# Performance work log

Measured on AMD Instinct MI355X. Metric: run time of the kernel, lower is better.

## Reference

```python
import jax, jax.numpy as jnp
import numpy as np

N_NODES = 50000
N_EDGES = 800000
NFEAT = 256
NHID = 128
NCLASS = 40
NLAYERS = 3


def setup_inputs() -> dict:
    key = jax.random.key(0)
    ks = jax.random.split(key, 8)
    x = jax.random.normal(ks[0], (N_NODES, NFEAT), dtype=jnp.float32)
    edge_src = jax.random.randint(ks[1], (N_EDGES,), 0, N_NODES, dtype=jnp.int32)
    edge_dst = jax.random.randint(ks[2], (N_EDGES,), 0, N_NODES, dtype=jnp.int32)
    # Kaiming-ish scaled params
    W_in = jax.random.normal(ks[3], (NFEAT, NHID), dtype=jnp.float32) / np.sqrt(NFEAT)
    b_in = jnp.zeros((NHID,), dtype=jnp.float32)
    W_mlps = jax.random.normal(ks[4], (NLAYERS, NHID, NHID), dtype=jnp.float32) / np.sqrt(NHID)
    b_mlps = jnp.zeros((NLAYERS, NHID), dtype=jnp.float32)
    W_out = jax.random.normal(ks[5], (NHID, NCLASS), dtype=jnp.float32) / np.sqrt(NHID)
    b_out = jnp.zeros((NCLASS,), dtype=jnp.float32)
    return {"x": x, "edge_src": edge_src, "edge_dst": edge_dst,
            "W_in": W_in, "b_in": b_in, "W_mlps": W_mlps, "b_mlps": b_mlps,
            "W_out": W_out, "b_out": b_out}


def reference(x, edge_src, edge_dst, W_in, b_in, W_mlps, b_mlps, W_out, b_out):
    # Dropout is identity in eval mode (training=False).
    n = x.shape[0]
    h = jax.nn.relu(x @ W_in + b_in)                       # [N, H]
    for i in range(NLAYERS):
        # GINConv with eps=0: h' = h + sum_{(s->d) in E} h[s] scattered to d
        agg = jax.ops.segment_sum(h[edge_src], edge_dst, num_segments=n)
        h = jax.nn.relu((h + agg) @ W_mlps[i] + b_mlps[i])  # [N, H]
    logits = h @ W_out + b_out                              # [N, C]
    return jax.nn.log_softmax(logits, axis=1)
```

## Files before the change

kernel.cpp:

```cpp
#include <hip/hip_runtime.h>
#include <math.h>

#define NHID 128
#define NFEAT 256
#define NCLASS 40

typedef __bf16 bf16x8 __attribute__((ext_vector_type(8)));
typedef __bf16 bf16x4 __attribute__((ext_vector_type(4)));
typedef float floatx4 __attribute__((ext_vector_type(4)));


__global__ __launch_bounds__(256) void bucket_hist(const int* __restrict__ edst,
                                                   int* __restrict__ bucket_counts,
                                                   int E, int nbuck) {
    __shared__ int lh[256];
    int tid = threadIdx.x;
    lh[tid] = 0;
    __syncthreads();
    int base = blockIdx.x * 4096;
#pragma unroll
    for (int k = 0; k < 16; ++k) {
        int e = base + k * 256 + tid;
        if (e < E) atomicAdd(&lh[edst[e] >> 8], 1);
    }
    __syncthreads();
    if (tid < nbuck && lh[tid]) atomicAdd(&bucket_counts[tid], lh[tid]);
}

__global__ __launch_bounds__(256) void bucket_scan(const int* __restrict__ counts,
                                                   int* __restrict__ start,
                                                   int* __restrict__ cursor,
                                                   int* __restrict__ row_ptr,
                                                   int nbuck, int E, int N) {
    __shared__ int lds[256];
    int tid = threadIdx.x;
    int v = (tid < nbuck) ? counts[tid] : 0;
    lds[tid] = v;
    __syncthreads();
    for (int off = 1; off < 256; off <<= 1) {
        int t = (tid >= off) ? lds[tid - off] : 0;
        __syncthreads();
        lds[tid] += t;
        __syncthreads();
    }
    int excl = lds[tid] - v;
    if (tid < nbuck) { start[tid] = excl; cursor[tid] = excl; }
    if (tid == 0) { start[nbuck] = E; row_ptr[N] = E; }
}

__global__ __launch_bounds__(256) void bucket_scatter(const int* __restrict__ esrc,
                                                      const int* __restrict__ edst,
                                                      int* __restrict__ cursor,
                                                      unsigned int* __restrict__ bdata,
                                                      int E, int nbuck) {
    __shared__ int lh[256];
    __shared__ int lbase[256];
    int tid = threadIdx.x;
    lh[tid] = 0;
    __syncthreads();
    int base = blockIdx.x * 4096;
    unsigned int recs[16];
    short bks[16];
    short lofs[16];
#pragma unroll
    for (int k = 0; k < 16; ++k) {
        int e = base + k * 256 + tid;
        bks[k] = -1;
        if (e < E) {
            int d = edst[e];
            int s = esrc[e];
            int b = d >> 8;
            recs[k] = ((unsigned int)(d & 255) << 16) | (unsigned int)s;
            bks[k] = (short)b;
            lofs[k] = (short)atomicAdd(&lh[b], 1);
        }
    }
    __syncthreads();
    if (tid < nbuck && lh[tid]) lbase[tid] = atomicAdd(&cursor[tid], lh[tid]);
    __syncthreads();
#pragma unroll
    for (int k = 0; k < 16; ++k) {
        if (bks[k] >= 0) bdata[lbase[bks[k]] + lofs[k]] = recs[k];
    }
}

__global__ __launch_bounds__(256) void bucket_finalize(const unsigned int* __restrict__ bdata,
                                                       const int* __restrict__ start,
                                                       int* __restrict__ row_ptr,
                                                       int* __restrict__ srcs,
                                                       int N) {
    __shared__ int hist[256];
    __shared__ int cur[256];
    int b = blockIdx.x;
    int tid = threadIdx.x;
    int s0 = start[b];
    int cnt = start[b + 1] - s0;
    hist[tid] = 0;
    __syncthreads();
    for (int i = tid; i < cnt; i += 256) atomicAdd(&hist[bdata[s0 + i] >> 16], 1);
    __syncthreads();
    int v0 = hist[tid];
    __syncthreads();
    for (int off = 1; off < 256; off <<= 1) {
        int t = (tid >= off) ? hist[tid - off] : 0;
        __syncthreads();
        hist[tid] += t;
        __syncthreads();
    }
    int excl = hist[tid] - v0;
    cur[tid] = excl;
    int node = b * 256 + tid;
    if (node < N) row_ptr[node] = s0 + excl;
    __syncthreads();
    for (int i = tid; i < cnt; i += 256) {
        unsigned int r = bdata[s0 + i];
        int p = atomicAdd(&cur[r >> 16], 1);
        srcs[s0 + p] = (int)(r & 0xffffu);
    }
}

template <int K>
__global__ __launch_bounds__(256) void transpose_split(const float* __restrict__ src,
                                                       __bf16* __restrict__ dhi,
                                                       __bf16* __restrict__ dlo, int total) {
    int i = blockIdx.x * 256 + threadIdx.x;
    if (i >= total) return;
    int per = 128 * K;
    int l = i / per;
    int r = i - l * per;
    int n = r / K;
    int k = r - n * K;
    float v = src[(size_t)l * per + (size_t)k * 128 + n];
    __bf16 hi = (__bf16)v;
    dhi[i] = hi;
    dlo[i] = (__bf16)(v - (float)hi);
}

__global__ __launch_bounds__(256) void aggregate_fused(const __bf16* __restrict__ hhi,
                                                       const __bf16* __restrict__ hlo,
                                                       const int* __restrict__ row_ptr,
                                                       const int* __restrict__ srcs,
                                                       __bf16* __restrict__ ohi,
                                                       __bf16* __restrict__ olo, int N) {
    int tid = threadIdx.x;
    int node = blockIdx.x * 4 + (tid >> 6);
    if (node >= N) return;
    int lane = tid & 63;
    int g = lane >> 4;
    int c = lane & 15;
    int beg = row_ptr[node];
    int end = row_ptr[node + 1];
    const bf16x8* hv = (const bf16x8*)hhi;

    bf16x8 sh = hv[(size_t)node * 16 + c];
    bf16x8 sl = ((const bf16x8*)hlo)[(size_t)node * 16 + c];

    float a[8], b2[8];
#pragma unroll
    for (int j = 0; j < 8; ++j) { a[j] = 0.f; b2[j] = 0.f; }

    int i = beg;
    for (; i + 16 <= end; i += 16) {
        int s0 = __builtin_nontemporal_load(&srcs[i + g]);
        int s1 = __builtin_nontemporal_load(&srcs[i + 4 + g]);
        int s2 = __builtin_nontemporal_load(&srcs[i + 8 + g]);
        int s3 = __builtin_nontemporal_load(&srcs[i + 12 + g]);
        bf16x8 v0 = hv[(size_t)s0 * 16 + c];
        bf16x8 v1 = hv[(size_t)s1 * 16 + c];
        bf16x8 v2 = hv[(size_t)s2 * 16 + c];
        bf16x8 v3 = hv[(size_t)s3 * 16 + c];
#pragma unroll
        for (int j = 0; j < 8; ++j) {
            a[j] += (float)v0[j] + (float)v2[j];
            b2[j] += (float)v1[j] + (float)v3[j];
        }
    }
    for (; i + 8 <= end; i += 8) {
        int s0 = __builtin_nontemporal_load(&srcs[i + g]);
        int s1 = __builtin_nontemporal_load(&srcs[i + 4 + g]);
        bf16x8 v0 = hv[(size_t)s0 * 16 + c];
        bf16x8 v1 = hv[(size_t)s1 * 16 + c];
#pragma unroll
        for (int j = 0; j < 8; ++j) { a[j] += (float)v0[j]; b2[j] += (float)v1[j]; }
    }
    for (; i < end; i += 4) {
        if (i + g < end) {
            int s = __builtin_nontemporal_load(&srcs[i + g]);
            bf16x8 v = hv[(size_t)s * 16 + c];
#pragma unroll
            for (int j = 0; j < 8; ++j) a[j] += (float)v[j];
        }
    }
#pragma unroll
    for (int j = 0; j < 8; ++j) a[j] += b2[j];
#pragma unroll
    for (int j = 0; j < 8; ++j) a[j] += __shfl_xor(a[j], 16);
#pragma unroll
    for (int j = 0; j < 8; ++j) a[j] += __shfl_xor(a[j], 32);

    if (g == 0) {
        bf16x8 whi, wlo;
#pragma unroll
        for (int j = 0; j < 8; ++j) {
            float v = a[j] + (float)sh[j] + (float)sl[j];
            __bf16 h = (__bf16)v;
            whi[j] = h;
            wlo[j] = (__bf16)(v - (float)h);
        }
        ((bf16x8*)ohi)[(size_t)node * 16 + c] = whi;
        ((bf16x8*)olo)[(size_t)node * 16 + c] = wlo;
    }
}

template <int MODE>
__global__ __launch_bounds__(256) void gemm_mfma(
    const float* __restrict__ Af, const __bf16* __restrict__ Ahi,
    const __bf16* __restrict__ Alo,
    const __bf16* __restrict__ Wthi, const __bf16* __restrict__ Wtlo,
    const float* __restrict__ bias, __bf16* __restrict__ Ohi,
    __bf16* __restrict__ Olo, int M, int K) {
    __shared__ __align__(16) char smem[49152];
    __bf16* sAhi = (__bf16*)smem;
    __bf16* sAlo = (__bf16*)(smem + 8192);
    __bf16* sWhi = (__bf16*)(smem + 16384);
    __bf16* sWlo = (__bf16*)(smem + 32768);

    int tid = threadIdx.x;
    int row0 = blockIdx.x * 64;
    int wave = tid >> 6;
    int l = tid & 63;
    int m16 = l & 15;
    int q = l >> 4;
    int axor = m16 & 7;
    int arow = wave * 16 + m16;

    floatx4 acc[8];
#pragma unroll
    for (int t = 0; t < 8; ++t) acc[t] = (floatx4){0.f, 0.f, 0.f, 0.f};

    for (int k0 = 0; k0 < K; k0 += 64) {
#pragma unroll
        for (int it = 0; it < 2; ++it) {
            int lin = it * 2048 + tid * 8;
            int row = lin >> 6, k = lin & 63;
            int g = min(row0 + row, M - 1);
            int off = row * 64 + (((k >> 3) ^ (row & 7)) << 3);
            if (MODE == 0) {
                float4 v0 = *(const float4*)&Af[(size_t)g * K + k0 + k];
                float4 v1 = *(const float4*)&Af[(size_t)g * K + k0 + k + 4];
                float s[8] = {v0.x, v0.y, v0.z, v0.w, v1.x, v1.y, v1.z, v1.w};
                bf16x8 shi, slo;
#pragma unroll
                for (int j = 0; j < 8; ++j) {
                    __bf16 h = (__bf16)s[j];
                    shi[j] = h;
                    slo[j] = (__bf16)(s[j] - (float)h);
                }
                *(bf16x8*)(sAhi + off) = shi;
                *(bf16x8*)(sAlo + off) = slo;
            } else {
                *(bf16x8*)(sAhi + off) = *(const bf16x8*)&Ahi[(size_t)g * 128 + k0 + k];
                *(bf16x8*)(sAlo + off) = *(const bf16x8*)&Alo[(size_t)g * 128 + k0 + k];
            }
        }
#pragma unroll
        for (int it = 0; it < 4; ++it) {
            int lin = it * 2048 + tid * 8;
            int n = lin >> 6, kk = lin & 63;
            int off = n * 64 + (((kk >> 3) ^ (n & 7)) << 3);
            *(bf16x8*)(sWhi + off) = *(const bf16x8*)&Wthi[(size_t)n * K + k0 + kk];
            *(bf16x8*)(sWlo + off) = *(const bf16x8*)&Wtlo[(size_t)n * K + k0 + kk];
        }
        __syncthreads();

#pragma unroll
        for (int s = 0; s < 2; ++s) {
            int sw = (((s * 4 + q) ^ axor) << 3);
            bf16x8 ahi = *(bf16x8*)(sAhi + arow * 64 + sw);
            bf16x8 alo = *(bf16x8*)(sAlo + arow * 64 + sw);
#pragma unroll
            for (int t = 0; t < 8; ++t) {
                int n = t * 16 + m16;
                bf16x8 bhi = *(bf16x8*)(sWhi + n * 64 + sw);
                bf16x8 blo = *(bf16x8*)(sWlo + n * 64 + sw);
                acc[t] = __builtin_amdgcn_mfma_f32_16x16x32_bf16(ahi, bhi, acc[t], 0, 0, 0);
                acc[t] = __builtin_amdgcn_mfma_f32_16x16x32_bf16(alo, bhi, acc[t], 0, 0, 0);
                acc[t] = __builtin_amdgcn_mfma_f32_16x16x32_bf16(ahi, blo, acc[t], 0, 0, 0);
            }
        }
        __syncthreads();
    }

    float* eps = (float*)(smem + 16384);
#pragma unroll
    for (int t = 0; t < 8; ++t) {
        int col = t * 16 + m16;
        float bb = bias[col];
#pragma unroll
        for (int i = 0; i < 4; ++i) {
            int row = wave * 16 + q * 4 + i;
            eps[row * 128 + col] = fmaxf(acc[t][i] + bb, 0.f);
        }
    }
    __syncthreads();
#pragma unroll
    for (int it = 0; it < 8; ++it) {
        int lin = it * 1024 + tid * 4;
        int row = lin >> 7, col = lin & 127;
        int g = row0 + row;
        if (g < M) {
            float4 v = *(float4*)(eps + lin);
            bf16x4 hi, lo;
            float vv[4] = {v.x, v.y, v.z, v.w};
#pragma unroll
            for (int j = 0; j < 4; ++j) {
                __bf16 h = (__bf16)vv[j];
                hi[j] = h;
                lo[j] = (__bf16)(vv[j] - (float)h);
            }
            *(bf16x4*)&Ohi[(size_t)g * 128 + col] = hi;
            *(bf16x4*)&Olo[(size_t)g * 128 + col] = lo;
        }
    }
}

__global__ __launch_bounds__(256) void out_logsoftmax(const __bf16* __restrict__ hhi,
                                                      const __bf16* __restrict__ hlo,
                                                      const float* __restrict__ Wout,
                                                      const float* __restrict__ bout,
                                                      float* __restrict__ out, int M) {
    __shared__ float sW[128 * NCLASS];
    __shared__ float sb[NCLASS];
    __shared__ float sH[32 * 132];
    int tid = threadIdx.x;
    for (int i = tid; i < 128 * NCLASS; i += 256) sW[i] = Wout[i];
    if (tid < NCLASS) sb[tid] = bout[tid];
    int row0 = blockIdx.x * 32;
#pragma unroll
    for (int it = 0; it < 4; ++it) {
        int i = tid * 4 + it * 1024;
        int r = i >> 7, k = i & 127;
        int rr = min(row0 + r, M - 1);
        uint2 uh = *(const uint2*)&hhi[(size_t)rr * 128 + k];
        uint2 ul = *(const uint2*)&hlo[(size_t)rr * 128 + k];
        sH[r * 132 + k + 0] = __uint_as_float(uh.x << 16) + __uint_as_float(ul.x << 16);
        sH[r * 132 + k + 1] = __uint_as_float(uh.x & 0xffff0000u) + __uint_as_float(ul.x & 0xffff0000u);
        sH[r * 132 + k + 2] = __uint_as_float(uh.y << 16) + __uint_as_float(ul.y << 16);
        sH[r * 132 + k + 3] = __uint_as_float(uh.y & 0xffff0000u) + __uint_as_float(ul.y & 0xffff0000u);
    }
    __syncthreads();

    int r = tid >> 3;
    int cg = tid & 7;
    float z[5];
#pragma unroll
    for (int j = 0; j < 5; ++j) z[j] = sb[cg * 5 + j];
    for (int k = 0; k < 128; ++k) {
        float a = sH[r * 132 + k];
#pragma unroll
        for (int j = 0; j < 5; ++j) z[j] += a * sW[k * NCLASS + cg * 5 + j];
    }
    float m = z[0];
#pragma unroll
    for (int j = 1; j < 5; ++j) m = fmaxf(m, z[j]);
    for (int off = 1; off < 8; off <<= 1) m = fmaxf(m, __shfl_xor(m, off));
    float s = 0.f;
#pragma unroll
    for (int j = 0; j < 5; ++j) s += expf(z[j] - m);
    for (int off = 1; off < 8; off <<= 1) s += __shfl_xor(s, off);
    float lse = m + logf(s);
    int row = row0 + r;
    if (row < M) {
#pragma unroll
        for (int j = 0; j < 5; ++j) out[(size_t)row * NCLASS + cg * 5 + j] = z[j] - lse;
    }
}

extern "C" void kernel_launch(void* const* d_in, const int* in_sizes, int n_in,
                              void* d_out, int out_size, void* d_ws, size_t ws_size,
                              hipStream_t stream) {
    const float* x      = (const float*)d_in[0];
    const int*   esrc   = (const int*)d_in[1];
    const int*   edst   = (const int*)d_in[2];
    const float* W_in   = (const float*)d_in[3];
    const float* b_in   = (const float*)d_in[4];
    const float* W_mlps = (const float*)d_in[5];
    const float* b_mlps = (const float*)d_in[6];
    const float* W_out  = (const float*)d_in[7];
    const float* b_out  = (const float*)d_in[8];
    float* out = (float*)d_out;

    int N = in_sizes[0] / NFEAT;
    int E = in_sizes[1];
    int nbuck = (N + 255) >> 8;

    char* ws = (char*)d_ws;
    size_t hb = (((size_t)N * NHID * sizeof(__bf16)) + 255) & ~(size_t)255;
    __bf16* h_hi_a = (__bf16*)ws;
    __bf16* h_lo_a = (__bf16*)(ws + hb);
    __bf16* h_hi_b = (__bf16*)(ws + 2 * hb);
    __bf16* h_lo_b = (__bf16*)(ws + 3 * hb);
    __bf16* sum_hi = (__bf16*)(ws + 4 * hb);
    __bf16* sum_lo = (__bf16*)(ws + 5 * hb);
    unsigned int* bdata = (unsigned int*)(ws + 4 * hb);
    char* ip = ws + 6 * hb;
    int* row_ptr = (int*)ip;  ip += (((size_t)(N + 1) * 4) + 255) & ~(size_t)255;
    int* srcs    = (int*)ip;  ip += (((size_t)E * 4) + 255) & ~(size_t)255;
    int* bucket_counts = (int*)ip;  ip += 1024;
    int* bucket_start  = (int*)ip;  ip += 1024;
    int* bucket_cursor = (int*)ip;  ip += 1024;
    __bf16* Wt_in_hi   = (__bf16*)ip;  ip += 128 * NFEAT * 2;
    __bf16* Wt_in_lo   = (__bf16*)ip;  ip += 128 * NFEAT * 2;
    __bf16* Wt_mlps_hi = (__bf16*)ip;  ip += 3 * 128 * NHID * 2;
    __bf16* Wt_mlps_lo = (__bf16*)ip;  ip += 3 * 128 * NHID * 2;

    int eb4 = (E + 4095) / 4096;

    hipMemsetAsync(bucket_counts, 0, 1024, stream);
    bucket_hist<<<eb4, 256, 0, stream>>>(edst, bucket_counts, E, nbuck);
    bucket_scan<<<1, 256, 0, stream>>>(bucket_counts, bucket_start, bucket_cursor,
                                       row_ptr, nbuck, E, N);
    bucket_scatter<<<eb4, 256, 0, stream>>>(esrc, edst, bucket_cursor, bdata, E, nbuck);
    bucket_finalize<<<nbuck, 256, 0, stream>>>(bdata, bucket_start, row_ptr, srcs, N);

    transpose_split<NFEAT><<<(128 * NFEAT + 255) / 256, 256, 0, stream>>>(
        W_in, Wt_in_hi, Wt_in_lo, 128 * NFEAT);
    transpose_split<NHID><<<(3 * 128 * NHID + 255) / 256, 256, 0, stream>>>(
        W_mlps, Wt_mlps_hi, Wt_mlps_lo, 3 * 128 * NHID);

    int gb = (N + 63) / 64;
    gemm_mfma<0><<<gb, 256, 0, stream>>>(x, (const __bf16*)nullptr, (const __bf16*)nullptr,
                                         Wt_in_hi, Wt_in_lo, b_in, h_hi_a, h_lo_a, N, NFEAT);

    __bf16* cur_hi = h_hi_a; __bf16* cur_lo = h_lo_a;
    __bf16* nxt_hi = h_hi_b; __bf16* nxt_lo = h_lo_b;
    for (int i = 0; i < 3; ++i) {
        aggregate_fused<<<(N + 3) / 4, 256, 0, stream>>>(cur_hi, cur_lo, row_ptr, srcs,
                                                         sum_hi, sum_lo, N);
        gemm_mfma<1><<<gb, 256, 0, stream>>>(
            (const float*)nullptr, sum_hi, sum_lo,
            Wt_mlps_hi + (size_t)i * 128 * NHID, Wt_mlps_lo + (size_t)i * 128 * NHID,
            b_mlps + (size_t)i * NHID, nxt_hi, nxt_lo, N, NHID);
        __bf16* t;
        t = cur_hi; cur_hi = nxt_hi; nxt_hi = t;
        t = cur_lo; cur_lo = nxt_lo; nxt_lo = t;
    }

    out_logsoftmax<<<(N + 31) / 32, 256, 0, stream>>>(cur_hi, cur_lo, W_out, b_out, out, N);
}
```

Measured before the change: 330.3 us.

## Fuse neighbor aggregation into MLP GEMM per 64-row block

Merges the per-layer aggregation kernel and the MFMA GEMM into one kernel. Each block first gathers and sums neighbor features for its 64 nodes straight into shared memory as hi/lo bf16, then runs the split-bf16 GEMM with bias and ReLU. This removes the intermediate sum buffer round-trip through global memory and one launch per layer. The cost is 64KB of shared memory per block, which lowers occupancy. It also changes the gather's parallelism from 4 nodes per block to 64 nodes processed sequentially, 16 per wave, which may expose gather latency.

```diff
diff --git a/kernel.cpp b/kernel.cpp
--- a/kernel.cpp
+++ b/kernel.cpp
@@ -136,86 +136,184 @@
     dlo[i] = (__bf16)(v - (float)hi);
 }
 
-__global__ __launch_bounds__(256) void aggregate_fused(const __bf16* __restrict__ hhi,
-                                                       const __bf16* __restrict__ hlo,
-                                                       const int* __restrict__ row_ptr,
-                                                       const int* __restrict__ srcs,
-                                                       __bf16* __restrict__ ohi,
-                                                       __bf16* __restrict__ olo, int N) {
-    int tid = threadIdx.x;
-    int node = blockIdx.x * 4 + (tid >> 6);
-    if (node >= N) return;
+__global__ __launch_bounds__(256) void gin_layer_fused(
+    const __bf16* __restrict__ hhi, const __bf16* __restrict__ hlo,
+    const int* __restrict__ row_ptr, const int* __restrict__ srcs,
+    const __bf16* __restrict__ Wthi, const __bf16* __restrict__ Wtlo,
+    const float* __restrict__ bias, __bf16* __restrict__ Ohi,
+    __bf16* __restrict__ Olo, int N) {
+    __shared__ __align__(16) char smem[65536];
+    __bf16* sAhi = (__bf16*)smem;
+    __bf16* sAlo = (__bf16*)(smem + 16384);
+    __bf16* sWhi = (__bf16*)(smem + 32768);
+    __bf16* sWlo = (__bf16*)(smem + 49152);
+
+    int tid = threadIdx.x;
+    int wave = tid >> 6;
     int lane = tid & 63;
+    int row0 = blockIdx.x * 64;
+
     int g = lane >> 4;
     int c = lane & 15;
-    int beg = row_ptr[node];
-    int end = row_ptr[node + 1];
     const bf16x8* hv = (const bf16x8*)hhi;
 
-    bf16x8 sh = hv[(size_t)node * 16 + c];
-    bf16x8 sl = ((const bf16x8*)hlo)[(size_t)node * 16 + c];
-
-    float a[8], b2[8];
-#pragma unroll
-    for (int j = 0; j < 8; ++j) { a[j] = 0.f; b2[j] = 0.f; }
-
-    int i = beg;
-    for (; i + 16 <= end; i += 16) {
-        int s0 = __builtin_nontemporal_load(&srcs[i + g]);
-        int s1 = __builtin_nontemporal_load(&srcs[i + 4 + g]);
-        int s2 = __builtin_nontemporal_load(&srcs[i + 8 + g]);
-        int s3 = __builtin_nontemporal_load(&srcs[i + 12 + g]);
-        bf16x8 v0 = hv[(size_t)s0 * 16 + c];
-        bf16x8 v1 = hv[(size_t)s1 * 16 + c];
-        bf16x8 v2 = hv[(size_t)s2 * 16 + c];
-        bf16x8 v3 = hv[(size_t)s3 * 16 + c];
-#pragma unroll
-        for (int j = 0; j < 8; ++j) {
-            a[j] += (float)v0[j] + (float)v2[j];
-            b2[j] += (float)v1[j] + (float)v3[j];
-        }
-    }
-    for (; i + 8 <= end; i += 8) {
-        int s0 = __builtin_nontemporal_load(&srcs[i + g]);
-        int s1 = __builtin_nontemporal_load(&srcs[i + 4 + g]);
-        bf16x8 v0 = hv[(size_t)s0 * 16 + c];
-        bf16x8 v1 = hv[(size_t)s1 * 16 + c];
-#pragma unroll
-        for (int j = 0; j < 8; ++j) { a[j] += (float)v0[j]; b2[j] += (float)v1[j]; }
-    }
-    for (; i < end; i += 4) {
-        if (i + g < end) {
-            int s = __builtin_nontemporal_load(&srcs[i + g]);
-            bf16x8 v = hv[(size_t)s * 16 + c];
-#pragma unroll
-            for (int j = 0; j < 8; ++j) a[j] += (float)v[j];
-        }
-    }
-#pragma unroll
-    for (int j = 0; j < 8; ++j) a[j] += b2[j];
-#pragma unroll
-    for (int j = 0; j < 8; ++j) a[j] += __shfl_xor(a[j], 16);
-#pragma unroll
-    for (int j = 0; j < 8; ++j) a[j] += __shfl_xor(a[j], 32);
-
-    if (g == 0) {
-        bf16x8 whi, wlo;
-#pragma unroll
-        for (int j = 0; j < 8; ++j) {
-            float v = a[j] + (float)sh[j] + (float)sl[j];
-            __bf16 h = (__bf16)v;
-            whi[j] = h;
-            wlo[j] = (__bf16)(v - (float)h);
-        }
-        ((bf16x8*)ohi)[(size_t)node * 16 + c] = whi;
-        ((bf16x8*)olo)[(size_t)node * 16 + c] = wlo;
-    }
-}
-
-template <int MODE>
-__global__ __launch_bounds__(256) void gemm_mfma(
-    const float* __restrict__ Af, const __bf16* __restrict__ Ahi,
-    const __bf16* __restrict__ Alo,
+    int rpl = 0;
+    {
+        int idx = row0 + wave * 16 + lane;
+        if (lane <= 16 && idx <= N) rpl = row_ptr[idx];
+    }
+
+    for (int t = 0; t < 16; ++t) {
+        int r = wave * 16 + t;
+        int node = row0 + r;
+        int off = r * 128 + ((c >> 3) << 6) + (((c & 7) ^ (r & 7)) << 3);
+        if (node >= N) {
+            if (g == 0) {
+                bf16x8 z;
+#pragma unroll
+                for (int j = 0; j < 8; ++j) z[j] = (__bf16)0.f;
+                *(bf16x8*)(sAhi + off) = z;
+                *(bf16x8*)(sAlo + off) = z;
+            }
+            continue;
+        }
+        int beg = __shfl(rpl, t);
+        int end = __shfl(rpl, t + 1);
+
+        bf16x8 sh = hv[(size_t)node * 16 + c];
+        bf16x8 sl = ((const bf16x8*)hlo)[(size_t)node * 16 + c];
+
+        float a[8], b2[8];
+#pragma unroll
+        for (int j = 0; j < 8; ++j) { a[j] = 0.f; b2[j] = 0.f; }
+
+        int i = beg;
+        for (; i + 16 <= end; i += 16) {
+            int s0 = __builtin_nontemporal_load(&srcs[i + g]);
+            int s1 = __builtin_nontemporal_load(&srcs[i + 4 + g]);
+            int s2 = __builtin_nontemporal_load(&srcs[i + 8 + g]);
+            int s3 = __builtin_nontemporal_load(&srcs[i + 12 + g]);
+            bf16x8 v0 = hv[(size_t)s0 * 16 + c];
+            bf16x8 v1 = hv[(size_t)s1 * 16 + c];
+            bf16x8 v2 = hv[(size_t)s2 * 16 + c];
+            bf16x8 v3 = hv[(size_t)s3 * 16 + c];
+#pragma unroll
+            for (int j = 0; j < 8; ++j) {
+                a[j] += (float)v0[j] + (float)v2[j];
+                b2[j] += (float)v1[j] + (float)v3[j];
+            }
+        }
+        for (; i + 8 <= end; i += 8) {
+            int s0 = __builtin_nontemporal_load(&srcs[i + g]);
+            int s1 = __builtin_nontemporal_load(&srcs[i + 4 + g]);
+            bf16x8 v0 = hv[(size_t)s0 * 16 + c];
+            bf16x8 v1 = hv[(size_t)s1 * 16 + c];
+#pragma unroll
+            for (int j = 0; j < 8; ++j) { a[j] += (float)v0[j]; b2[j] += (float)v1[j]; }
+        }
+        for (; i < end; i += 4) {
+            if (i + g < end) {
+                int s = __builtin_nontemporal_load(&srcs[i + g]);
+                bf16x8 v = hv[(size_t)s * 16 + c];
+#pragma unroll
+                for (int j = 0; j < 8; ++j) a[j] += (float)v[j];
+            }
+        }
+#pragma unroll
+        for (int j = 0; j < 8; ++j) a[j] += b2[j];
+#pragma unroll
+        for (int j = 0; j < 8; ++j) a[j] += __shfl_xor(a[j], 16);
+#pragma unroll
+        for (int j = 0; j < 8; ++j) a[j] += __shfl_xor(a[j], 32);
+
+        if (g == 0) {
+            bf16x8 whi, wlo;
+#pragma unroll
+            for (int j = 0; j < 8; ++j) {
+                float v = a[j] + (float)sh[j] + (float)sl[j];
+                __bf16 h = (__bf16)v;
+                whi[j] = h;
+                wlo[j] = (__bf16)(v - (float)h);
+            }
+            *(bf16x8*)(sAhi + off) = whi;
+            *(bf16x8*)(sAlo + off) = wlo;
+        }
+    }
+    __syncthreads();
+
+    int m16 = lane & 15;
+    int q = lane >> 4;
+    int axor = m16 & 7;
+    int arow = wave * 16 + m16;
+
+    floatx4 acc[8];
+#pragma unroll
+    for (int t = 0; t < 8; ++t) acc[t] = (floatx4){0.f, 0.f, 0.f, 0.f};
+
+    for (int k0 = 0; k0 < 128; k0 += 64) {
+#pragma unroll
+        for (int it = 0; it < 4; ++it) {
+            int lin = it * 2048 + tid * 8;
+            int n = lin >> 6, kk = lin & 63;
+            int off = n * 64 + (((kk >> 3) ^ (n & 7)) << 3);
+            *(bf16x8*)(sWhi + off) = *(const bf16x8*)&Wthi[(size_t)n * 128 + k0 + kk];
+            *(bf16x8*)(sWlo + off) = *(const bf16x8*)&Wtlo[(size_t)n * 128 + k0 + kk];
+        }
+        __syncthreads();
+
+#pragma unroll
+        for (int s = 0; s < 2; ++s) {
+            int sw = (((s * 4 + q) ^ axor) << 3);
+            bf16x8 ahi = *(bf16x8*)(sAhi + arow * 128 + k0 + sw);
+            bf16x8 alo = *(bf16x8*)(sAlo + arow * 128 + k0 + sw);
+#pragma unroll
+            for (int t = 0; t < 8; ++t) {
+                int n = t * 16 + m16;
+                bf16x8 bhi = *(bf16x8*)(sWhi + n * 64 + sw);
+                bf16x8 blo = *(bf16x8*)(sWlo + n * 64 + sw);
+                acc[t] = __builtin_amdgcn_mfma_f32_16x16x32_bf16(ahi, bhi, acc[t], 0, 0, 0);
+                acc[t] = __builtin_amdgcn_mfma_f32_16x16x32_bf16(alo, bhi, acc[t], 0, 0, 0);
+                acc[t] = __builtin_amdgcn_mfma_f32_16x16x32_bf16(ahi, blo, acc[t], 0, 0, 0);
+            }
+        }
+        __syncthreads();
+    }
+
+    float* eps = (float*)(smem + 32768);
+#pragma unroll
+    for (int t = 0; t < 8; ++t) {
+        int col = t * 16 + m16;
+        float bb = bias[col];
+#pragma unroll
+        for (int i = 0; i < 4; ++i) {
+            int row = wave * 16 + q * 4 + i;
+            eps[row * 128 + col] = fmaxf(acc[t][i] + bb, 0.f);
+        }
+    }
+    __syncthreads();
+#pragma unroll
+    for (int it = 0; it < 8; ++it) {
+        int lin = it * 1024 + tid * 4;
+        int row = lin >> 7, col = lin & 127;
+        int gg = row0 + row;
+        if (gg < N) {
+            float4 v = *(float4*)(eps + lin);
+            bf16x4 hi, lo;
+            float vv[4] = {v.x, v.y, v.z, v.w};
+#pragma unroll
+            for (int j = 0; j < 4; ++j) {
+                __bf16 h = (__bf16)vv[j];
+                hi[j] = h;
+                lo[j] = (__bf16)(vv[j] - (float)h);
+            }
+            *(bf16x4*)&Ohi[(size_t)gg * 128 + col] = hi;
+            *(bf16x4*)&Olo[(size_t)gg * 128 + col] = lo;
+        }
+    }
+}
+
+__global__ __launch_bounds__(256) void gemm_in(
+    const float* __restrict__ Af,
     const __bf16* __restrict__ Wthi, const __bf16* __restrict__ Wtlo,
     const float* __restrict__ bias, __bf16* __restrict__ Ohi,
     __bf16* __restrict__ Olo, int M, int K) {
@@ -245,23 +343,18 @@
             int row = lin >> 6, k = lin & 63;
             int g = min(row0 + row, M - 1);
             int off = row * 64 + (((k >> 3) ^ (row & 7)) << 3);
-            if (MODE == 0) {
-                float4 v0 = *(const float4*)&Af[(size_t)g * K + k0 + k];
-                float4 v1 = *(const float4*)&Af[(size_t)g * K + k0 + k + 4];
-                float s[8] = {v0.x, v0.y, v0.z, v0.w, v1.x, v1.y, v1.z, v1.w};
-                bf16x8 shi, slo;
-#pragma unroll
-                for (int j = 0; j < 8; ++j) {
-                    __bf16 h = (__bf16)s[j];
-                    shi[j] = h;
-                    slo[j] = (__bf16)(s[j] - (float)h);
-                }
-                *(bf16x8*)(sAhi + off) = shi;
-                *(bf16x8*)(sAlo + off) = slo;
-            } else {
-                *(bf16x8*)(sAhi + off) = *(const bf16x8*)&Ahi[(size_t)g * 128 + k0 + k];
-                *(bf16x8*)(sAlo + off) = *(const bf16x8*)&Alo[(size_t)g * 128 + k0 + k];
-            }
+            float4 v0 = *(const float4*)&Af[(size_t)g * K + k0 + k];
+            float4 v1 = *(const float4*)&Af[(size_t)g * K + k0 + k + 4];
+            float s[8] = {v0.x, v0.y, v0.z, v0.w, v1.x, v1.y, v1.z, v1.w};
+            bf16x8 shi, slo;
+#pragma unroll
+            for (int j = 0; j < 8; ++j) {
+                __bf16 h = (__bf16)s[j];
+                shi[j] = h;
+                slo[j] = (__bf16)(s[j] - (float)h);
+            }
+            *(bf16x8*)(sAhi + off) = shi;
+            *(bf16x8*)(sAlo + off) = slo;
         }
 #pragma unroll
         for (int it = 0; it < 4; ++it) {
@@ -400,8 +493,6 @@
     __bf16* h_lo_a = (__bf16*)(ws + hb);
     __bf16* h_hi_b = (__bf16*)(ws + 2 * hb);
     __bf16* h_lo_b = (__bf16*)(ws + 3 * hb);
-    __bf16* sum_hi = (__bf16*)(ws + 4 * hb);
-    __bf16* sum_lo = (__bf16*)(ws + 5 * hb);
     unsigned int* bdata = (unsigned int*)(ws + 4 * hb);
     char* ip = ws + 6 * hb;
     int* row_ptr = (int*)ip;  ip += (((size_t)(N + 1) * 4) + 255) & ~(size_t)255;
@@ -429,18 +520,15 @@
         W_mlps, Wt_mlps_hi, Wt_mlps_lo, 3 * 128 * NHID);
 
     int gb = (N + 63) / 64;
-    gemm_mfma<0><<<gb, 256, 0, stream>>>(x, (const __bf16*)nullptr, (const __bf16*)nullptr,
-                                         Wt_in_hi, Wt_in_lo, b_in, h_hi_a, h_lo_a, N, NFEAT);
+    gemm_in<<<gb, 256, 0, stream>>>(x, Wt_in_hi, Wt_in_lo, b_in, h_hi_a, h_lo_a, N, NFEAT);
 
     __bf16* cur_hi = h_hi_a; __bf16* cur_lo = h_lo_a;
     __bf16* nxt_hi = h_hi_b; __bf16* nxt_lo = h_lo_b;
     for (int i = 0; i < 3; ++i) {
-        aggregate_fused<<<(N + 3) / 4, 256, 0, stream>>>(cur_hi, cur_lo, row_ptr, srcs,
-                                                         sum_hi, sum_lo, N);
-        gemm_mfma<1><<<gb, 256, 0, stream>>>(
-            (const float*)nullptr, sum_hi, sum_lo,
+        gin_layer_fused<<<gb, 256, 0, stream>>>(
+            cur_hi, cur_lo, row_ptr, srcs,
             Wt_mlps_hi + (size_t)i * 128 * NHID, Wt_mlps_lo + (size_t)i * 128 * NHID,
-            b_mlps + (size_t)i * NHID, nxt_hi, nxt_lo, N, NHID);
+            b_mlps + (size_t)i * NHID, nxt_hi, nxt_lo, N);
         __bf16* t;
         t = cur_hi; cur_hi = nxt_hi; nxt_hi = t;
         t = cur_lo; cur_lo = nxt_lo; nxt_lo = t;
```

Result: slower. 448.9 us (+35.9%).

## Fuse last MLP GEMM with output projection and log-softmax; merge weight transposes

Applied to the files above, without the earlier changes.

Adds a gemm_out kernel that runs the final layer's MFMA GEMM with split-bf16 precision, applies bias and ReLU, and then computes the output logits and log-softmax from shared memory in one pass. This avoids writing and re-reading the final hidden state as hi/lo bf16 and removes one kernel launch. The two weight transpose/split kernels are also merged into a single launch. The fused kernel uses about 56KB of shared memory, which may lower occupancy for the GEMM part.

```diff
diff --git a/kernel.cpp b/kernel.cpp
--- a/kernel.cpp
+++ b/kernel.cpp
@@ -119,21 +119,32 @@
     }
 }
 
-template <int K>
-__global__ __launch_bounds__(256) void transpose_split(const float* __restrict__ src,
-                                                       __bf16* __restrict__ dhi,
-                                                       __bf16* __restrict__ dlo, int total) {
+__global__ __launch_bounds__(256) void transpose_split_all(
+    const float* __restrict__ Win, const float* __restrict__ Wmlps,
+    __bf16* __restrict__ dInHi, __bf16* __restrict__ dInLo,
+    __bf16* __restrict__ dMlHi, __bf16* __restrict__ dMlLo) {
+    const int TOT_IN = 128 * NFEAT;
+    const int TOT_ML = 3 * 128 * NHID;
     int i = blockIdx.x * 256 + threadIdx.x;
-    if (i >= total) return;
-    int per = 128 * K;
-    int l = i / per;
-    int r = i - l * per;
-    int n = r / K;
-    int k = r - n * K;
-    float v = src[(size_t)l * per + (size_t)k * 128 + n];
-    __bf16 hi = (__bf16)v;
-    dhi[i] = hi;
-    dlo[i] = (__bf16)(v - (float)hi);
+    if (i < TOT_IN) {
+        int n = i / NFEAT;
+        int k = i - n * NFEAT;
+        float v = Win[(size_t)k * 128 + n];
+        __bf16 h = (__bf16)v;
+        dInHi[i] = h;
+        dInLo[i] = (__bf16)(v - (float)h);
+    } else if (i < TOT_IN + TOT_ML) {
+        int r = i - TOT_IN;
+        int per = 128 * NHID;
+        int l = r / per;
+        int rr = r - l * per;
+        int n = rr / NHID;
+        int k = rr - n * NHID;
+        float v = Wmlps[(size_t)l * per + (size_t)k * 128 + n];
+        __bf16 h = (__bf16)v;
+        dMlHi[r] = h;
+        dMlLo[r] = (__bf16)(v - (float)h);
+    }
 }
 
 __global__ __launch_bounds__(256) void aggregate_fused(const __bf16* __restrict__ hhi,
@@ -324,55 +335,111 @@
     }
 }
 
-__global__ __launch_bounds__(256) void out_logsoftmax(const __bf16* __restrict__ hhi,
-                                                      const __bf16* __restrict__ hlo,
-                                                      const float* __restrict__ Wout,
-                                                      const float* __restrict__ bout,
-                                                      float* __restrict__ out, int M) {
-    __shared__ float sW[128 * NCLASS];
-    __shared__ float sb[NCLASS];
-    __shared__ float sH[32 * 132];
-    int tid = threadIdx.x;
-    for (int i = tid; i < 128 * NCLASS; i += 256) sW[i] = Wout[i];
+__global__ __launch_bounds__(256) void gemm_out(
+    const __bf16* __restrict__ Ahi, const __bf16* __restrict__ Alo,
+    const __bf16* __restrict__ Wthi, const __bf16* __restrict__ Wtlo,
+    const float* __restrict__ bias,
+    const float* __restrict__ Wout, const float* __restrict__ bout,
+    float* __restrict__ out, int M) {
+    __shared__ __align__(16) char smem[57344];
+    __bf16* sAhi = (__bf16*)smem;
+    __bf16* sAlo = (__bf16*)(smem + 8192);
+    __bf16* sWhi = (__bf16*)(smem + 16384);
+    __bf16* sWlo = (__bf16*)(smem + 32768);
+
+    int tid = threadIdx.x;
+    int row0 = blockIdx.x * 64;
+    int wave = tid >> 6;
+    int l = tid & 63;
+    int m16 = l & 15;
+    int q = l >> 4;
+    int axor = m16 & 7;
+    int arow = wave * 16 + m16;
+
+    floatx4 acc[8];
+#pragma unroll
+    for (int t = 0; t < 8; ++t) acc[t] = (floatx4){0.f, 0.f, 0.f, 0.f};
+
+    for (int k0 = 0; k0 < 128; k0 += 64) {
+#pragma unroll
+        for (int it = 0; it < 2; ++it) {
+            int lin = it * 2048 + tid * 8;
+            int row = lin >> 6, k = lin & 63;
+            int g = min(row0 + row, M - 1);
+            int off = row * 64 + (((k >> 3) ^ (row & 7)) << 3);
+            *(bf16x8*)(sAhi + off) = *(const bf16x8*)&Ahi[(size_t)g * 128 + k0 + k];
+            *(bf16x8*)(sAlo + off) = *(const bf16x8*)&Alo[(size_t)g * 128 + k0 + k];
+        }
+#pragma unroll
+        for (int it = 0; it < 4; ++it) {
+            int lin = it * 2048 + tid * 8;
+            int n = lin >> 6, kk = lin & 63;
+            int off = n * 64 + (((kk >> 3) ^ (n & 7)) << 3);
+            *(bf16x8*)(sWhi + off) = *(const bf16x8*)&Wthi[(size_t)n * 128 + k0 + kk];
+            *(bf16x8*)(sWlo + off) = *(const bf16x8*)&Wtlo[(size_t)n * 128 + k0 + kk];
+        }
+        __syncthreads();
+
+#pragma unroll
+        for (int s = 0; s < 2; ++s) {
+            int sw = (((s * 4 + q) ^ axor) << 3);
+            bf16x8 ahi = *(bf16x8*)(sAhi + arow * 64 + sw);
+            bf16x8 alo = *(bf16x8*)(sAlo + arow * 64 + sw);
+#pragma unroll
+            for (int t = 0; t < 8; ++t) {
+                int n = t * 16 + m16;
+                bf16x8 bhi = *(bf16x8*)(sWhi + n * 64 + sw);
+                bf16x8 blo = *(bf16x8*)(sWlo + n * 64 + sw);
+                acc[t] = __builtin_amdgcn_mfma_f32_16x16x32_bf16(ahi, bhi, acc[t], 0, 0, 0);
+                acc[t] = __builtin_amdgcn_mfma_f32_16x16x32_bf16(alo, bhi, acc[t], 0, 0, 0);
+                acc[t] = __builtin_amdgcn_mfma_f32_16x16x32_bf16(ahi, blo, acc[t], 0, 0, 0);
+            }
+        }
+        __syncthreads();
+    }
+
+    float* eps = (float*)smem;
+    float* sWo = (float*)(smem + 34816);
+    float* sb  = (float*)(smem + 55296);
+#pragma unroll
+    for (int t = 0; t < 8; ++t) {
+        int col = t * 16 + m16;
+        float bb = bias[col];
+#pragma unroll
+        for (int i = 0; i < 4; ++i) {
+            int row = wave * 16 + q * 4 + i;
+            eps[row * 132 + col] = fmaxf(acc[t][i] + bb, 0.f);
+        }
+    }
+    for (int i = tid; i < 128 * NCLASS; i += 256) sWo[i] = Wout[i];
     if (tid < NCLASS) sb[tid] = bout[tid];
-    int row0 = blockIdx.x * 32;
-#pragma unroll
-    for (int it = 0; it < 4; ++it) {
-        int i = tid * 4 + it * 1024;
-        int r = i >> 7, k = i & 127;
-        int rr = min(row0 + r, M - 1);
-        uint2 uh = *(const uint2*)&hhi[(size_t)rr * 128 + k];
-        uint2 ul = *(const uint2*)&hlo[(size_t)rr * 128 + k];
-        sH[r * 132 + k + 0] = __uint_as_float(uh.x << 16) + __uint_as_float(ul.x << 16);
-        sH[r * 132 + k + 1] = __uint_as_float(uh.x & 0xffff0000u) + __uint_as_float(ul.x & 0xffff0000u);
-        sH[r * 132 + k + 2] = __uint_as_float(uh.y << 16) + __uint_as_float(ul.y << 16);
-        sH[r * 132 + k + 3] = __uint_as_float(uh.y & 0xffff0000u) + __uint_as_float(ul.y & 0xffff0000u);
-    }
-    __syncthreads();
-
-    int r = tid >> 3;
-    int cg = tid & 7;
-    float z[5];
-#pragma unroll
-    for (int j = 0; j < 5; ++j) z[j] = sb[cg * 5 + j];
+    __syncthreads();
+
+    int r = tid >> 2;
+    int cg = tid & 3;
+    float z[10];
+#pragma unroll
+    for (int j = 0; j < 10; ++j) z[j] = sb[cg * 10 + j];
     for (int k = 0; k < 128; ++k) {
-        float a = sH[r * 132 + k];
-#pragma unroll
-        for (int j = 0; j < 5; ++j) z[j] += a * sW[k * NCLASS + cg * 5 + j];
+        float a = eps[r * 132 + k];
+#pragma unroll
+        for (int j = 0; j < 10; ++j) z[j] += a * sWo[k * NCLASS + cg * 10 + j];
     }
     float m = z[0];
 #pragma unroll
-    for (int j = 1; j < 5; ++j) m = fmaxf(m, z[j]);
-    for (int off = 1; off < 8; off <<= 1) m = fmaxf(m, __shfl_xor(m, off));
+    for (int j = 1; j < 10; ++j) m = fmaxf(m, z[j]);
+    m = fmaxf(m, __shfl_xor(m, 1));
+    m = fmaxf(m, __shfl_xor(m, 2));
     float s = 0.f;
 #pragma unroll
-    for (int j = 0; j < 5; ++j) s += expf(z[j] - m);
-    for (int off = 1; off < 8; off <<= 1) s += __shfl_xor(s, off);
+    for (int j = 0; j < 10; ++j) s += expf(z[j] - m);
+    s += __shfl_xor(s, 1);
+    s += __shfl_xor(s, 2);
     float lse = m + logf(s);
     int row = row0 + r;
     if (row < M) {
 #pragma unroll
-        for (int j = 0; j < 5; ++j) out[(size_t)row * NCLASS + cg * 5 + j] = z[j] - lse;
+        for (int j = 0; j < 10; ++j) out[(size_t)row * NCLASS + cg * 10 + j] = z[j] - lse;
     }
 }
 
@@ -423,10 +490,8 @@
     bucket_scatter<<<eb4, 256, 0, stream>>>(esrc, edst, bucket_cursor, bdata, E, nbuck);
     bucket_finalize<<<nbuck, 256, 0, stream>>>(bdata, bucket_start, row_ptr, srcs, N);
 
-    transpose_split<NFEAT><<<(128 * NFEAT + 255) / 256, 256, 0, stream>>>(
-        W_in, Wt_in_hi, Wt_in_lo, 128 * NFEAT);
-    transpose_split<NHID><<<(3 * 128 * NHID + 255) / 256, 256, 0, stream>>>(
-        W_mlps, Wt_mlps_hi, Wt_mlps_lo, 3 * 128 * NHID);
+    transpose_split_all<<<(128 * NFEAT + 3 * 128 * NHID + 255) / 256, 256, 0, stream>>>(
+        W_in, W_mlps, Wt_in_hi, Wt_in_lo, Wt_mlps_hi, Wt_mlps_lo);
 
     int gb = (N + 63) / 64;
     gemm_mfma<0><<<gb, 256, 0, stream>>>(x, (const __bf16*)nullptr, (const __bf16*)nullptr,
@@ -434,7 +499,7 @@
 
     __bf16* cur_hi = h_hi_a; __bf16* cur_lo = h_lo_a;
     __bf16* nxt_hi = h_hi_b; __bf16* nxt_lo = h_lo_b;
-    for (int i = 0; i < 3; ++i) {
+    for (int i = 0; i < 2; ++i) {
         aggregate_fused<<<(N + 3) / 4, 256, 0, stream>>>(cur_hi, cur_lo, row_ptr, srcs,
                                                          sum_hi, sum_lo, N);
         gemm_mfma<1><<<gb, 256, 0, stream>>>(
@@ -446,5 +511,11 @@
         t = cur_lo; cur_lo = nxt_lo; nxt_lo = t;
     }
 
-    out_logsoftmax<<<(N + 31) / 32, 256, 0, stream>>>(cur_hi, cur_lo, W_out, b_out, out, N);
-}
+    aggregate_fused<<<(N + 3) / 4, 256, 0, stream>>>(cur_hi, cur_lo, row_ptr, srcs,
+                                                     sum_hi, sum_lo, N);
+    gemm_out<<<gb, 256, 0, stream>>>(sum_hi, sum_lo,
+                                     Wt_mlps_hi + (size_t)2 * 128 * NHID,
+                                     Wt_mlps_lo + (size_t)2 * 128 * NHID,
+                                     b_mlps + (size_t)2 * NHID,
+                                     W_out, b_out, out, N);
+}
```

Measured after the change: 324.1 us. Within noise of the previous version (-1.9%).
